# Performance work log

Hardware: AMD Instinct MI355X
Metric: run time of the kernel (lower is better)

Reference implementation:

```python
import jax, jax.numpy as jnp
import numpy as np

K = 20          # neighbors
BN_EPS = 1e-5


def _knn_idx(x, k):
    """x: [B, C, N] -> idx of k nearest neighbors [B, N, k] (by squared distance, self included)."""
    xx = jnp.sum(x * x, axis=1)                       # [B, N]
    inner = jnp.einsum('bcn,bcm->bnm', x, x)          # [B, N, N]
    neg_sqdist = 2.0 * inner - xx[:, :, None] - xx[:, None, :]
    return jax.lax.top_k(neg_sqdist, k)[1]            # [B, N, k]


def _graph_feature(x, k):
    """x: [B, C, N] -> edge features cat(x_j - x_i, x_i): [B, 2C, N, k]."""
    idx = _knn_idx(x, k)                              # [B, N, k]
    xT = x.transpose(0, 2, 1)                         # [B, N, C]
    nbrs = jax.vmap(lambda xt, ii: xt[ii])(xT, idx)   # [B, N, k, C] gather
    center = xT[:, :, None, :]                        # [B, N, 1, C]
    feat = jnp.concatenate(
        [nbrs - center, jnp.broadcast_to(center, nbrs.shape)], axis=-1)  # [B, N, k, 2C]
    return feat.transpose(0, 3, 1, 2)                 # [B, 2C, N, k]


def _conv_bn_lrelu(feat, W, gamma, beta, mean, var):
    """1x1 Conv2d (no bias) + BatchNorm (given stats) + LeakyReLU(0.2). feat: [B, Cin, N, k]."""
    y = jnp.einsum('oc,bcnk->bonk', W, feat)
    scale = (gamma / jnp.sqrt(var + BN_EPS))[None, :, None, None]
    y = (y - mean[None, :, None, None]) * scale + beta[None, :, None, None]
    return jnp.where(y > 0, y, 0.2 * y)


def setup_inputs() -> dict:
    key = jax.random.key(0)
    ks = list(jax.random.split(key, 32))
    B, N = 8, 1024
    f32 = jnp.float32

    def w(kk, o, i):
        return jax.random.normal(kk, (o, i), dtype=f32) / np.sqrt(i)

    def bn(k1, k2, k3, k4, c):
        g = jax.random.uniform(k1, (c,), dtype=f32, minval=0.5, maxval=1.5)
        b = jax.random.normal(k2, (c,), dtype=f32) * 0.05
        m = jax.random.normal(k3, (c,), dtype=f32) * 0.05
        v = jax.random.uniform(k4, (c,), dtype=f32, minval=0.5, maxval=1.5)
        return g, b, m, v

    x = jax.random.normal(ks[0], (B, N, 3), dtype=f32)
    W0 = w(ks[1], 64, 6);    g0, b0, m0, v0 = bn(ks[2], ks[3], ks[4], ks[5], 64)
    W1 = w(ks[6], 128, 128); g1, b1, m1, v1 = bn(ks[7], ks[8], ks[9], ks[10], 128)
    W2 = w(ks[11], 256, 256); g2, b2, m2, v2 = bn(ks[12], ks[13], ks[14], ks[15], 256)
    Wf = w(ks[16], 512, 896); gf, bf, mf, vf = bn(ks[17], ks[18], ks[19], ks[20], 512)
    We = w(ks[21], 256, 512)
    return dict(x=x,
                W0=W0, g0=g0, b0=b0, m0=m0, v0=v0,
                W1=W1, g1=g1, b1=b1, m1=m1, v1=v1,
                W2=W2, g2=g2, b2=b2, m2=m2, v2=v2,
                Wf=Wf, gf=gf, bf=bf, mf=mf, vf=vf,
                We=We)


def reference(x, W0, g0, b0, m0, v0, W1, g1, b1, m1, v1,
              W2, g2, b2, m2, v2, Wf, gf, bf, mf, vf, We):
    h = x.transpose(0, 2, 1)                          # [B, 3, N]
    outs = []
    for (W, g, b, m, v) in ((W0, g0, b0, m0, v0),
                            (W1, g1, b1, m1, v1),
                            (W2, g2, b2, m2, v2)):
        gfeat = _graph_feature(h, K)                  # [B, 2C, N, k]
        y = _conv_bn_lrelu(gfeat, W, g, b, m, v)      # [B, Cout, N, k]
        h = y.mean(axis=-1)                           # max-free EdgeConv pool over k
        outs.append(h)
    cat = jnp.concatenate(outs, axis=1)               # [B, 448, N]
    gfeat = _graph_feature(cat, K)                    # [B, 896, N, k]
    y = _conv_bn_lrelu(gfeat, Wf, gf, bf, mf, vf)     # [B, 512, N, k]
    pooled = y.mean(axis=-1).mean(axis=-1)            # [B, 512] (pool over k then N)
    return pooled @ We.T                              # [B, num_features]
```

## Files before the change

kernel.cpp:

```cpp
#include <hip/hip_runtime.h>
#include <cstdint>

#define KNN 20
#define BV 8
#define NV 1024

template <int CTRL>
__device__ __forceinline__ unsigned dppmax(unsigned x) {
    unsigned m = (unsigned)__builtin_amdgcn_update_dpp((int)x, (int)x, CTRL, 0xf, 0xf, false);
    return (x > m) ? x : m;
}
template <int CTRL>
__device__ __forceinline__ unsigned dppmin(unsigned x) {
    unsigned m = (unsigned)__builtin_amdgcn_update_dpp((int)x, (int)x, CTRL, 0xf, 0xf, false);
    return (x < m) ? x : m;
}
__device__ __forceinline__ unsigned wave_max_u32(unsigned x) {
    x = dppmax<0xB1>(x); x = dppmax<0x4E>(x); x = dppmax<0x141>(x);
    x = dppmax<0x140>(x); x = dppmax<0x142>(x); x = dppmax<0x143>(x);
    return (unsigned)__builtin_amdgcn_readlane((int)x, 63);
}
__device__ __forceinline__ unsigned wave_min_u32(unsigned x) {
    x = dppmin<0xB1>(x); x = dppmin<0x4E>(x); x = dppmin<0x141>(x);
    x = dppmin<0x140>(x); x = dppmin<0x142>(x); x = dppmin<0x143>(x);
    return (unsigned)__builtin_amdgcn_readlane((int)x, 63);
}

__global__ __launch_bounds__(256) void k_transpose(const float* __restrict__ x, float* __restrict__ hx) {
    int id = blockIdx.x * 256 + threadIdx.x;
    if (id >= BV * 3 * NV) return;
    int n = id % NV;
    int c = (id / NV) % 3;
    int b = id / (3 * NV);
    hx[id] = x[(b * NV + n) * 3 + c];
}

__global__ __launch_bounds__(256) void k_xx(const float* __restrict__ h, float* __restrict__ xx,
                                            int C, int bstride) {
    int id = blockIdx.x * 256 + threadIdx.x;
    int n = id % NV, b = id / NV;
    if (b >= BV) return;
    const float* hp = h + (size_t)b * bstride + n;
    float s = 0.f;
    for (int c = 0; c < C; ++c) { float v = hp[(size_t)c * NV]; s += v * v; }
    xx[b * NV + n] = s;
}

__global__ __launch_bounds__(512) void k_knn(const float* __restrict__ h, const float* __restrict__ xx,
                                             int C, int bstride, int* __restrict__ idx) {
    __shared__ float Bs[8][1024];
    const int b = blockIdx.x, i0 = blockIdx.y * 32;
    const int t = threadIdx.x, lane = t & 63, w = t >> 6;
    const int irow = i0 + w * 4;
    float acc[4][16] = {};
    const float* hb = h + (size_t)b * bstride;

    for (int c0 = 0; c0 < C; c0 += 8) {
        __syncthreads();
#pragma unroll
        for (int r = 0; r < 4; ++r) {
            int e = r * 512 + t;
            int cc = e >> 8, jj = e & 255;
            float4 v = make_float4(0.f, 0.f, 0.f, 0.f);
            if (c0 + cc < C) v = *(const float4*)&hb[(size_t)(c0 + cc) * NV + jj * 4];
            *(float4*)&Bs[cc][jj * 4] = v;
        }
        __syncthreads();
#pragma unroll
        for (int c = 0; c < 8; ++c) {
            float4 arv = *(const float4*)&Bs[c][irow];
            float ar[4] = {arv.x, arv.y, arv.z, arv.w};
            float br[16];
#pragma unroll
            for (int g = 0; g < 4; ++g) {
                float4 bv = *(const float4*)&Bs[c][g * 256 + (lane << 2)];
                br[g * 4 + 0] = bv.x; br[g * 4 + 1] = bv.y;
                br[g * 4 + 2] = bv.z; br[g * 4 + 3] = bv.w;
            }
#pragma unroll
            for (int a = 0; a < 4; ++a)
#pragma unroll
                for (int q = 0; q < 16; ++q) acc[a][q] += ar[a] * br[q];
        }
    }

    const float* xb = xx + b * NV;
    float xxj[16];
#pragma unroll
    for (int g = 0; g < 4; ++g) {
        float4 xv = *(const float4*)&xb[g * 256 + (lane << 2)];
        xxj[g * 4 + 0] = xv.x; xxj[g * 4 + 1] = xv.y;
        xxj[g * 4 + 2] = xv.z; xxj[g * 4 + 3] = xv.w;
    }
#pragma unroll
    for (int a = 0; a < 4; ++a) {
        float xi = xb[irow + a];
#pragma unroll
        for (int q = 0; q < 16; ++q) acc[a][q] = 2.f * acc[a][q] - xi - xxj[q];
    }

    int* opb = idx + ((size_t)(b * NV + irow)) * KNN;
#pragma unroll 1
    for (int s = 0; s < KNN; ++s) {
#pragma unroll
        for (int a = 0; a < 4; ++a) {
            float bv = acc[a][0]; int bq = 0;
#pragma unroll
            for (int q = 1; q < 16; ++q)
                if (acc[a][q] > bv) { bv = acc[a][q]; bq = q; }
            unsigned u = __float_as_uint(bv);
            unsigned su = ((int)u < 0) ? ~u : (u | 0x80000000u);
            int myj = ((bq >> 2) << 8) | (lane << 2) | (bq & 3);
            unsigned gmax = wave_max_u32(su);
            unsigned cand = (su == gmax) ? (unsigned)myj : 0xFFFFFFFFu;
            int j = (int)wave_min_u32(cand);
            if (lane == 0) opb[a * KNN + s] = j;
            int wq = (((j >> 2) & 63) == lane) ? (((j >> 8) << 2) | (j & 3)) : 99;
#pragma unroll
            for (int q = 0; q < 16; ++q)
                if (wq == q) acc[a][q] = -3.4e38f;
        }
    }
}

__global__ __launch_bounds__(256) void k_pack(const float* __restrict__ W, float* __restrict__ wb,
                                              int C, int O) {
    int id = blockIdx.x * 256 + threadIdx.x;
    if (id >= 2 * O * C) return;
    int c = id % C, o = (id / C) % O, half = id / (C * O);
    float wl = W[(size_t)o * 2 * C + c];
    wb[id] = half ? (W[(size_t)o * 2 * C + C + c] - wl) : wl;
}

__global__ __launch_bounds__(256) void k_gemm(const float* __restrict__ A, int astride,
                                              const float* __restrict__ h, int bstride, int C,
                                              float* __restrict__ out, int O) {
    __shared__ float Ws[8][64], Hs[8][128];
    const int b = blockIdx.z, o0 = blockIdx.y * 64, n0 = blockIdx.x * 128;
    const int t = threadIdx.x, tx = t & 15, ty = t >> 4;
    float acc[4][8] = {};
    const float* hb = h + (size_t)b * bstride;
    for (int c0 = 0; c0 < C; c0 += 8) {
#pragma unroll
        for (int q = 0; q < 2; ++q) {
            int e = t + q * 256;
            int oo = e >> 3, cc = e & 7;
            Ws[cc][oo] = ((c0 + cc) < C) ? A[(size_t)(o0 + oo) * astride + c0 + cc] : 0.f;
        }
        {
            int cc = t >> 5, nn4 = t & 31;
            float4 v = make_float4(0.f, 0.f, 0.f, 0.f);
            if (c0 + cc < C) v = *(const float4*)&hb[(size_t)(c0 + cc) * NV + n0 + nn4 * 4];
            *(float4*)&Hs[cc][nn4 * 4] = v;
        }
        __syncthreads();
#pragma unroll
        for (int c = 0; c < 8; ++c) {
            float4 wv = *(const float4*)&Ws[c][ty * 4];
            float ar[4] = {wv.x, wv.y, wv.z, wv.w};
            float br[8];
            float4 h0 = *(const float4*)&Hs[c][tx * 4];
            float4 h1 = *(const float4*)&Hs[c][64 + tx * 4];
            br[0] = h0.x; br[1] = h0.y; br[2] = h0.z; br[3] = h0.w;
            br[4] = h1.x; br[5] = h1.y; br[6] = h1.z; br[7] = h1.w;
#pragma unroll
            for (int a = 0; a < 4; ++a)
#pragma unroll
                for (int q = 0; q < 8; ++q) acc[a][q] += ar[a] * br[q];
        }
        __syncthreads();
    }
#pragma unroll
    for (int a = 0; a < 4; ++a) {
        int o = o0 + ty * 4 + a;
        float* outp = out + ((size_t)b * O + o) * NV + n0;
        float4 s0 = make_float4(acc[a][0], acc[a][1], acc[a][2], acc[a][3]);
        float4 s1 = make_float4(acc[a][4], acc[a][5], acc[a][6], acc[a][7]);
        *(float4*)&outp[tx * 4] = s0;
        *(float4*)&outp[64 + tx * 4] = s1;
    }
}

__global__ __launch_bounds__(256) void k_edge(const float* __restrict__ pd,
                                              const int* __restrict__ idx,
                                              const float* __restrict__ ga, const float* __restrict__ be,
                                              const float* __restrict__ mu, const float* __restrict__ va,
                                              float* __restrict__ out, int out_bstride, int O) {
    const int n = blockIdx.x * 256 + threadIdx.x;
    const int o = blockIdx.y, b = blockIdx.z;
    const float a  = ga[o] / sqrtf(va[o] + 1e-5f);
    const float c0 = be[o] - mu[o] * a;
    const float* pb = pd + ((size_t)b * 2 * O + o) * NV;
    const float dv  = pd[((size_t)b * 2 * O + O + o) * NV + n];
    const int* ip   = idx + ((size_t)b * NV + n) * KNN;
    float s = 0.f;
#pragma unroll
    for (int k = 0; k < KNN; ++k) {
        int j = ip[k];
        float y = fmaf(a, pb[j] + dv, c0);
        s += (y > 0.f) ? y : 0.2f * y;
    }
    out[(size_t)b * out_bstride + (size_t)o * NV + n] = s * (1.f / KNN);
}

__global__ __launch_bounds__(256) void k_pool(const float* __restrict__ hf, float* __restrict__ pooled) {
    const int o = blockIdx.x, b = blockIdx.y;
    const float* hp = hf + ((size_t)b * 512 + o) * NV;
    float s = 0.f;
    for (int i = threadIdx.x; i < NV; i += 256) s += hp[i];
#pragma unroll
    for (int off = 32; off > 0; off >>= 1) s += __shfl_down(s, off, 64);
    __shared__ float red[4];
    if ((threadIdx.x & 63) == 0) red[threadIdx.x >> 6] = s;
    __syncthreads();
    if (threadIdx.x == 0)
        pooled[(size_t)b * 512 + o] = (red[0] + red[1] + red[2] + red[3]) * (1.f / NV);
}

__global__ __launch_bounds__(256) void k_final(const float* __restrict__ pooled, const float* __restrict__ We,
                                               float* __restrict__ out) {
    const int j = threadIdx.x, b = blockIdx.x;
    __shared__ float ps[512];
    for (int o = threadIdx.x; o < 512; o += 256) ps[o] = pooled[b * 512 + o];
    __syncthreads();
    float s = 0.f;
    for (int o = 0; o < 512; ++o) s += ps[o] * We[(size_t)j * 512 + o];
    out[b * 256 + j] = s;
}

extern "C" void kernel_launch(void* const* d_in, const int* in_sizes, int n_in,
                              void* d_out, int out_size, void* d_ws, size_t ws_size,
                              hipStream_t stream) {
    const float* x  = (const float*)d_in[0];
    const float* W0 = (const float*)d_in[1];
    const float* g0 = (const float*)d_in[2];
    const float* b0 = (const float*)d_in[3];
    const float* m0 = (const float*)d_in[4];
    const float* v0 = (const float*)d_in[5];
    const float* W1 = (const float*)d_in[6];
    const float* g1 = (const float*)d_in[7];
    const float* b1 = (const float*)d_in[8];
    const float* m1 = (const float*)d_in[9];
    const float* v1 = (const float*)d_in[10];
    const float* W2 = (const float*)d_in[11];
    const float* g2 = (const float*)d_in[12];
    const float* b2 = (const float*)d_in[13];
    const float* m2 = (const float*)d_in[14];
    const float* v2 = (const float*)d_in[15];
    const float* Wf = (const float*)d_in[16];
    const float* gf = (const float*)d_in[17];
    const float* bf = (const float*)d_in[18];
    const float* mf = (const float*)d_in[19];
    const float* vf = (const float*)d_in[20];
    const float* We = (const float*)d_in[21];

    float* ws = (float*)d_ws;
    float* hx     = ws;
    float* cat    = hx + 24576;
    float* xx     = cat + 3670016;
    int*   idx    = (int*)(xx + 8192);
    float* pd     = (float*)(idx + 163840);
    float* wb     = pd + 8388608;
    float* hf     = wb + 458752;
    float* pooled = hf + 4194304;

    k_transpose<<<96, 256, 0, stream>>>(x, hx);

    auto run_layer = [&](const float* h, int C, int bstride, const float* W,
                         const float* g, const float* be, const float* m, const float* v,
                         int O, float* outp, int obstride) {
        k_xx<<<32, 256, 0, stream>>>(h, xx, C, bstride);
        k_knn<<<dim3(8, 32), 512, 0, stream>>>(h, xx, C, bstride, idx);
        int pn = 2 * O * C;
        k_pack<<<(pn + 255) / 256, 256, 0, stream>>>(W, wb, C, O);
        k_gemm<<<dim3(8, 2 * O / 64, 8), 256, 0, stream>>>(wb, C, h, bstride, C, pd, 2 * O);
        k_edge<<<dim3(4, O, 8), 256, 0, stream>>>(pd, idx, g, be, m, v, outp, obstride, O);
    };

    run_layer(hx, 3, 3 * NV, W0, g0, b0, m0, v0, 64, cat, 448 * NV);
    run_layer(cat, 64, 448 * NV, W1, g1, b1, m1, v1, 128, cat + 64 * NV, 448 * NV);
    run_layer(cat + 64 * NV, 128, 448 * NV, W2, g2, b2, m2, v2, 256, cat + 192 * NV, 448 * NV);
    run_layer(cat, 448, 448 * NV, Wf, gf, bf, mf, vf, 512, hf, 512 * NV);

    k_pool<<<dim3(512, 8), 256, 0, stream>>>(hf, pooled);
    k_final<<<8, 256, 0, stream>>>(pooled, We, (float*)d_out);
}
```

Baseline: 840.6 us.

## Split kNN into smaller blocks with tree-based argmax selection

The kNN kernel now uses 256-thread blocks that each own 8 query rows, with two rows per wave instead of four. The grid grows from 256 to 1024 blocks, giving more parallelism across the GPU. The per-lane argmax over 16 candidates becomes a pairwise tree reduction that shortens the dependency chain, and the winner-invalidation test is simplified to reuse the lane's own candidate. In exchange, each block reloads the full column tile of the point set, so total shared-memory loads and global reads per row go up.

```diff
diff --git a/kernel.cpp b/kernel.cpp
--- a/kernel.cpp
+++ b/kernel.cpp
@@ -46,20 +46,20 @@
     xx[b * NV + n] = s;
 }
 
-__global__ __launch_bounds__(512) void k_knn(const float* __restrict__ h, const float* __restrict__ xx,
-                                             int C, int bstride, int* __restrict__ idx) {
+__global__ __launch_bounds__(256, 4) void k_knn(const float* __restrict__ h, const float* __restrict__ xx,
+                                                int C, int bstride, int* __restrict__ idx) {
     __shared__ float Bs[8][1024];
-    const int b = blockIdx.x, i0 = blockIdx.y * 32;
+    const int b = blockIdx.y, i0 = blockIdx.x * 8;
     const int t = threadIdx.x, lane = t & 63, w = t >> 6;
-    const int irow = i0 + w * 4;
-    float acc[4][16] = {};
+    const int irow = i0 + w * 2;
+    float acc[2][16] = {};
     const float* hb = h + (size_t)b * bstride;
 
     for (int c0 = 0; c0 < C; c0 += 8) {
         __syncthreads();
 #pragma unroll
-        for (int r = 0; r < 4; ++r) {
-            int e = r * 512 + t;
+        for (int r = 0; r < 8; ++r) {
+            int e = r * 256 + t;
             int cc = e >> 8, jj = e & 255;
             float4 v = make_float4(0.f, 0.f, 0.f, 0.f);
             if (c0 + cc < C) v = *(const float4*)&hb[(size_t)(c0 + cc) * NV + jj * 4];
@@ -68,8 +68,8 @@
         __syncthreads();
 #pragma unroll
         for (int c = 0; c < 8; ++c) {
-            float4 arv = *(const float4*)&Bs[c][irow];
-            float ar[4] = {arv.x, arv.y, arv.z, arv.w};
+            float2 arv = *(const float2*)&Bs[c][irow];
+            float ar[2] = {arv.x, arv.y};
             float br[16];
 #pragma unroll
             for (int g = 0; g < 4; ++g) {
@@ -78,7 +78,7 @@
                 br[g * 4 + 2] = bv.z; br[g * 4 + 3] = bv.w;
             }
 #pragma unroll
-            for (int a = 0; a < 4; ++a)
+            for (int a = 0; a < 2; ++a)
 #pragma unroll
                 for (int q = 0; q < 16; ++q) acc[a][q] += ar[a] * br[q];
         }
@@ -93,7 +93,7 @@
         xxj[g * 4 + 2] = xv.z; xxj[g * 4 + 3] = xv.w;
     }
 #pragma unroll
-    for (int a = 0; a < 4; ++a) {
+    for (int a = 0; a < 2; ++a) {
         float xi = xb[irow + a];
 #pragma unroll
         for (int q = 0; q < 16; ++q) acc[a][q] = 2.f * acc[a][q] - xi - xxj[q];
@@ -103,11 +103,32 @@
 #pragma unroll 1
     for (int s = 0; s < KNN; ++s) {
 #pragma unroll
-        for (int a = 0; a < 4; ++a) {
-            float bv = acc[a][0]; int bq = 0;
-#pragma unroll
-            for (int q = 1; q < 16; ++q)
-                if (acc[a][q] > bv) { bv = acc[a][q]; bq = q; }
+        for (int a = 0; a < 2; ++a) {
+            float v0[8]; int q0[8];
+#pragma unroll
+            for (int i = 0; i < 8; ++i) {
+                bool g = acc[a][2 * i + 1] > acc[a][2 * i];
+                v0[i] = g ? acc[a][2 * i + 1] : acc[a][2 * i];
+                q0[i] = g ? 2 * i + 1 : 2 * i;
+            }
+            float v1[4]; int q1[4];
+#pragma unroll
+            for (int i = 0; i < 4; ++i) {
+                bool g = v0[2 * i + 1] > v0[2 * i];
+                v1[i] = g ? v0[2 * i + 1] : v0[2 * i];
+                q1[i] = g ? q0[2 * i + 1] : q0[2 * i];
+            }
+            float v2[2]; int q2[2];
+#pragma unroll
+            for (int i = 0; i < 2; ++i) {
+                bool g = v1[2 * i + 1] > v1[2 * i];
+                v2[i] = g ? v1[2 * i + 1] : v1[2 * i];
+                q2[i] = g ? q1[2 * i + 1] : q1[2 * i];
+            }
+            bool gf = v2[1] > v2[0];
+            float bv = gf ? v2[1] : v2[0];
+            int bq = gf ? q2[1] : q2[0];
+
             unsigned u = __float_as_uint(bv);
             unsigned su = ((int)u < 0) ? ~u : (u | 0x80000000u);
             int myj = ((bq >> 2) << 8) | (lane << 2) | (bq & 3);
@@ -115,7 +136,7 @@
             unsigned cand = (su == gmax) ? (unsigned)myj : 0xFFFFFFFFu;
             int j = (int)wave_min_u32(cand);
             if (lane == 0) opb[a * KNN + s] = j;
-            int wq = (((j >> 2) & 63) == lane) ? (((j >> 8) << 2) | (j & 3)) : 99;
+            int wq = (myj == j && su == gmax) ? bq : 99;
 #pragma unroll
             for (int q = 0; q < 16; ++q)
                 if (wq == q) acc[a][q] = -3.4e38f;
@@ -270,7 +291,7 @@
                          const float* g, const float* be, const float* m, const float* v,
                          int O, float* outp, int obstride) {
         k_xx<<<32, 256, 0, stream>>>(h, xx, C, bstride);
-        k_knn<<<dim3(8, 32), 512, 0, stream>>>(h, xx, C, bstride, idx);
+        k_knn<<<dim3(128, 8), 256, 0, stream>>>(h, xx, C, bstride, idx);
         int pn = 2 * O * C;
         k_pack<<<(pn + 255) / 256, 256, 0, stream>>>(W, wb, C, O);
         k_gemm<<<dim3(8, 2 * O / 64, 8), 256, 0, stream>>>(wb, C, h, bstride, C, pd, 2 * O);
```

Result: slower. 887.1 us (+5.5%).

## Split kNN columns into two halves per block and merge partial top-k lists

Applied to the files above, without the earlier changes.

The kNN kernel now handles 512 candidate columns per block instead of 1024, which doubles the grid to 512 blocks and halves the per-thread accumulator registers, with launch bounds raised to target more waves. Each half writes its sorted top-20 (ordered key and index) to scratch, and a new merge kernel combines the two lists per row. The per-step argmax is rewritten as a tree reduction. The aim is better occupancy and parallelism on the latency-bound selection loop, at the cost of an extra launch, extra global traffic and redundant loads of the A rows.

```diff
diff --git a/kernel.cpp b/kernel.cpp
--- a/kernel.cpp
+++ b/kernel.cpp
@@ -46,80 +46,122 @@
     xx[b * NV + n] = s;
 }
 
-__global__ __launch_bounds__(512) void k_knn(const float* __restrict__ h, const float* __restrict__ xx,
-                                             int C, int bstride, int* __restrict__ idx) {
-    __shared__ float Bs[8][1024];
-    const int b = blockIdx.x, i0 = blockIdx.y * 32;
+__global__ __launch_bounds__(512, 4) void k_knn(const float* __restrict__ h, const float* __restrict__ xx,
+                                                int C, int bstride,
+                                                unsigned* __restrict__ sval, int* __restrict__ sidx) {
+    __shared__ float Bs[8][512];
+    __shared__ float As[8][32];
+    const int tile = blockIdx.x, half = blockIdx.y, b = blockIdx.z;
+    const int i0 = tile * 32, jbase = half * 512;
     const int t = threadIdx.x, lane = t & 63, w = t >> 6;
     const int irow = i0 + w * 4;
-    float acc[4][16] = {};
+    float acc[4][8] = {};
     const float* hb = h + (size_t)b * bstride;
 
     for (int c0 = 0; c0 < C; c0 += 8) {
         __syncthreads();
 #pragma unroll
-        for (int r = 0; r < 4; ++r) {
+        for (int r = 0; r < 2; ++r) {
             int e = r * 512 + t;
-            int cc = e >> 8, jj = e & 255;
+            int cc = e >> 7, g = e & 127;
             float4 v = make_float4(0.f, 0.f, 0.f, 0.f);
-            if (c0 + cc < C) v = *(const float4*)&hb[(size_t)(c0 + cc) * NV + jj * 4];
-            *(float4*)&Bs[cc][jj * 4] = v;
+            if (c0 + cc < C) v = *(const float4*)&hb[(size_t)(c0 + cc) * NV + jbase + g * 4];
+            *(float4*)&Bs[cc][g * 4] = v;
+        }
+        if (t < 64) {
+#pragma unroll
+            for (int r = 0; r < 4; ++r) {
+                int e = r * 64 + t;
+                int cc = e >> 5, ii = e & 31;
+                As[cc][ii] = (c0 + cc < C) ? hb[(size_t)(c0 + cc) * NV + i0 + ii] : 0.f;
+            }
         }
         __syncthreads();
 #pragma unroll
         for (int c = 0; c < 8; ++c) {
-            float4 arv = *(const float4*)&Bs[c][irow];
+            float4 arv = *(const float4*)&As[c][w * 4];
             float ar[4] = {arv.x, arv.y, arv.z, arv.w};
-            float br[16];
-#pragma unroll
-            for (int g = 0; g < 4; ++g) {
-                float4 bv = *(const float4*)&Bs[c][g * 256 + (lane << 2)];
-                br[g * 4 + 0] = bv.x; br[g * 4 + 1] = bv.y;
-                br[g * 4 + 2] = bv.z; br[g * 4 + 3] = bv.w;
-            }
+            float4 b0 = *(const float4*)&Bs[c][lane * 8];
+            float4 b1 = *(const float4*)&Bs[c][lane * 8 + 4];
+            float br[8] = {b0.x, b0.y, b0.z, b0.w, b1.x, b1.y, b1.z, b1.w};
 #pragma unroll
             for (int a = 0; a < 4; ++a)
 #pragma unroll
-                for (int q = 0; q < 16; ++q) acc[a][q] += ar[a] * br[q];
+                for (int q = 0; q < 8; ++q) acc[a][q] += ar[a] * br[q];
         }
     }
 
     const float* xb = xx + b * NV;
-    float xxj[16];
-#pragma unroll
-    for (int g = 0; g < 4; ++g) {
-        float4 xv = *(const float4*)&xb[g * 256 + (lane << 2)];
-        xxj[g * 4 + 0] = xv.x; xxj[g * 4 + 1] = xv.y;
-        xxj[g * 4 + 2] = xv.z; xxj[g * 4 + 3] = xv.w;
-    }
+    float4 x0 = *(const float4*)&xb[jbase + lane * 8];
+    float4 x1 = *(const float4*)&xb[jbase + lane * 8 + 4];
+    float xxj[8] = {x0.x, x0.y, x0.z, x0.w, x1.x, x1.y, x1.z, x1.w};
 #pragma unroll
     for (int a = 0; a < 4; ++a) {
         float xi = xb[irow + a];
 #pragma unroll
-        for (int q = 0; q < 16; ++q) acc[a][q] = 2.f * acc[a][q] - xi - xxj[q];
-    }
-
-    int* opb = idx + ((size_t)(b * NV + irow)) * KNN;
+        for (int q = 0; q < 8; ++q) acc[a][q] = 2.f * acc[a][q] - xi - xxj[q];
+    }
+
 #pragma unroll 1
     for (int s = 0; s < KNN; ++s) {
 #pragma unroll
         for (int a = 0; a < 4; ++a) {
-            float bv = acc[a][0]; int bq = 0;
-#pragma unroll
-            for (int q = 1; q < 16; ++q)
-                if (acc[a][q] > bv) { bv = acc[a][q]; bq = q; }
+            float v0[4]; int q0[4];
+#pragma unroll
+            for (int i = 0; i < 4; ++i) {
+                bool g = acc[a][2 * i + 1] > acc[a][2 * i];
+                v0[i] = g ? acc[a][2 * i + 1] : acc[a][2 * i];
+                q0[i] = g ? 2 * i + 1 : 2 * i;
+            }
+            float v1[2]; int q1[2];
+#pragma unroll
+            for (int i = 0; i < 2; ++i) {
+                bool g = v0[2 * i + 1] > v0[2 * i];
+                v1[i] = g ? v0[2 * i + 1] : v0[2 * i];
+                q1[i] = g ? q0[2 * i + 1] : q0[2 * i];
+            }
+            bool gf = v1[1] > v1[0];
+            float bv = gf ? v1[1] : v1[0];
+            int bq = gf ? q1[1] : q1[0];
+
             unsigned u = __float_as_uint(bv);
             unsigned su = ((int)u < 0) ? ~u : (u | 0x80000000u);
-            int myj = ((bq >> 2) << 8) | (lane << 2) | (bq & 3);
+            int myj = jbase + lane * 8 + bq;
             unsigned gmax = wave_max_u32(su);
             unsigned cand = (su == gmax) ? (unsigned)myj : 0xFFFFFFFFu;
             int j = (int)wave_min_u32(cand);
-            if (lane == 0) opb[a * KNN + s] = j;
-            int wq = (((j >> 2) & 63) == lane) ? (((j >> 8) << 2) | (j & 3)) : 99;
-#pragma unroll
-            for (int q = 0; q < 16; ++q)
+            if (lane == 0) {
+                size_t o = ((size_t)(b * NV + irow + a) * 2 + half) * KNN + s;
+                sval[o] = gmax;
+                sidx[o] = j;
+            }
+            int wq = (myj == j && su == gmax) ? bq : 99;
+#pragma unroll
+            for (int q = 0; q < 8; ++q)
                 if (wq == q) acc[a][q] = -3.4e38f;
         }
+    }
+}
+
+__global__ __launch_bounds__(256) void k_merge(const unsigned* __restrict__ sval,
+                                               const int* __restrict__ sidx,
+                                               int* __restrict__ idx) {
+    int row = blockIdx.x * 256 + threadIdx.x;
+    if (row >= BV * NV) return;
+    const unsigned* v0 = sval + (size_t)row * 2 * KNN;
+    const unsigned* v1 = v0 + KNN;
+    const int* i0p = sidx + (size_t)row * 2 * KNN;
+    const int* i1p = i0p + KNN;
+    int* op = idx + (size_t)row * KNN;
+    int a = 0, c = 0;
+#pragma unroll
+    for (int s = 0; s < KNN; ++s) {
+        unsigned va = v0[a], vb = v1[c];
+        int ia = i0p[a], ib = i1p[c];
+        bool take0 = (va > vb) || (va == vb && ia < ib);
+        op[s] = take0 ? ia : ib;
+        a += take0 ? 1 : 0;
+        c += take0 ? 0 : 1;
     }
 }
 
@@ -263,6 +305,8 @@
     float* wb     = pd + 8388608;
     float* hf     = wb + 458752;
     float* pooled = hf + 4194304;
+    unsigned* sval = (unsigned*)(pooled + 4096);
+    int*      sidx = (int*)(sval + 327680);
 
     k_transpose<<<96, 256, 0, stream>>>(x, hx);
 
@@ -270,7 +314,8 @@
                          const float* g, const float* be, const float* m, const float* v,
                          int O, float* outp, int obstride) {
         k_xx<<<32, 256, 0, stream>>>(h, xx, C, bstride);
-        k_knn<<<dim3(8, 32), 512, 0, stream>>>(h, xx, C, bstride, idx);
+        k_knn<<<dim3(32, 2, 8), 512, 0, stream>>>(h, xx, C, bstride, sval, sidx);
+        k_merge<<<32, 256, 0, stream>>>(sval, sidx, idx);
         int pn = 2 * O * C;
         k_pack<<<(pn + 255) / 256, 256, 0, stream>>>(W, wb, C, O);
         k_gemm<<<dim3(8, 2 * O / 64, 8), 256, 0, stream>>>(wb, C, h, bstride, C, pd, 2 * O);
```

Result: slower. 890.0 us (+5.9%).
